# Kernel tuning notes

Hardware: AMD Instinct MI355X
Metric: run time of the kernel (lower is better)

## Reference

```python
import jax, jax.numpy as jnp
import numpy as np

BOX = 8.0  # side length of the box points are sampled in
N_POINTS = 12288
N_BINS_TARGET = 10


def setup_inputs() -> dict:
    key = jax.random.key(0)
    k1, k2 = jax.random.split(key)
    pc = jax.random.uniform(k1, (N_POINTS, 3), dtype=jnp.float32) * BOX
    target_rdf = jax.random.uniform(k2, (N_BINS_TARGET,), dtype=jnp.float32) * 2.0
    return {"reconstructed_pc": pc, "target_rdf": target_rdf, "r_max": 10, "dr": 1.0}


def _calculate_rdf(pc, r_max, dr):
    # pc: [N, 3]. r_max, dr are static Python scalars.
    n = pc.shape[0]
    nbins = int(round(float(r_max) / float(dr)))  # len(arange(0, r_max+dr, dr)) - 1
    # Pairwise Euclidean distances via the Gram-matrix trick (same math as torch.cdist p=2).
    sq = jnp.sum(pc * pc, axis=1)                               # [N]
    d2 = sq[:, None] + sq[None, :] - 2.0 * (pc @ pc.T)          # [N, N]
    d = jnp.sqrt(jnp.maximum(d2, 0.0)).ravel()                  # [N*N]
    # torch.histc(bins=nbins, min=0, max=r_max): uniform bins, max value inclusive in last bin.
    idx = jnp.clip(jnp.floor(d / dr).astype(jnp.int32), 0, nbins - 1)
    w = (d <= r_max).astype(jnp.float32)                        # d >= 0 always holds
    hist = jax.ops.segment_sum(w, idx, num_segments=nbins)      # [nbins]
    r_mid = (jnp.arange(nbins, dtype=jnp.float32) + 0.5) * dr
    density = n / (4.0 / 3.0 * jnp.pi * float(r_max) ** 3)
    ideal_counts = 4.0 * jnp.pi * r_mid ** 2 * dr * density * n
    rdf = hist / ideal_counts
    rdf = jnp.where(jnp.isnan(rdf), 0.0, rdf)
    return rdf, r_mid


def reference(reconstructed_pc, target_rdf, r_max, dr):
    rdf, _ = _calculate_rdf(reconstructed_pc, r_max, dr)
    m = min(int(target_rdf.shape[0]), int(rdf.shape[0]))
    diff = rdf[:m] - target_rdf[:m]
    return jnp.mean(diff * diff)
```

## Files before the change

### kernel.cpp

```cpp
#include <hip/hip_runtime.h>


#define BLOCK    256
#define NB       10
#define SLOT     16
#define FP32_SAT 16777216u

__device__ __forceinline__ int row_start(int r, int T) {
    return r * T - ((r * (r - 1)) >> 1);
}

template <bool DIAG>
__device__ __forceinline__ void tile_loop(const float4* __restrict__ sj,
                                          float sqi, float m2x, float m2y, float m2z,
                                          int tid, unsigned int* c)
{
    for (int jc = 0; jc < BLOCK; jc += 32) {
        unsigned long long cnt = 0ull;
        #pragma unroll
        for (int jj = 0; jj < 32; ++jj) {
            const int j = jc + jj;
            float4 p = sj[j];
            float d2 = sqi + p.w;
            d2 = fmaf(m2x, p.x, d2);
            d2 = fmaf(m2y, p.y, d2);
            d2 = fmaf(m2z, p.z, d2);
            if (DIAG) d2 = (j > tid) ? d2 : 3.0e30f;
            float d = __builtin_amdgcn_sqrtf(d2);
            unsigned int b = (unsigned int)d;
            b = min(b, 10u);
            cnt += 1ull << (b * 6u);
        }
        #pragma unroll
        for (int k = 0; k < NB; ++k)
            c[k] += (unsigned int)(cnt >> (6 * k)) & 63u;
    }
}

__global__ __launch_bounds__(BLOCK) void rdf_hist_kernel(
    const float* __restrict__ pc, const int* __restrict__ rmaxp,
    const float* __restrict__ drp, unsigned int* __restrict__ part,
    int n, int T)
{
    __shared__ float4 sj[BLOCK];
    __shared__ unsigned int sacc[NB];

    const int tid = threadIdx.x;
    const int bid = (int)blockIdx.x;

    const float tf = (float)T;
    float disc = (2.f*tf + 1.f)*(2.f*tf + 1.f) - 8.f*(float)bid;
    int ti = (int)((2.f*tf + 1.f - sqrtf(disc)) * 0.5f);
    ti = max(0, min(ti, T - 1));
    while (ti > 0 && row_start(ti, T) > bid) --ti;
    while (row_start(ti + 1, T) <= bid) ++ti;
    const int tj = ti + (bid - row_start(ti, T));

    const float inv_dr = 1.0f / (*drp);

    if (tid < NB) sacc[tid] = 0u;

    {
        const int j = tj * BLOCK + tid;
        float x = -3.0e4f, y = -3.0e4f, z = -3.0e4f;
        if (j < n) { x = pc[3*j] * inv_dr; y = pc[3*j+1] * inv_dr; z = pc[3*j+2] * inv_dr; }
        sj[tid] = make_float4(x, y, z, x*x + y*y + z*z);
    }
    const int i = ti * BLOCK + tid;
    float xi = 3.0e4f, yi = 3.0e4f, zi = 3.0e4f;
    if (i < n) { xi = pc[3*i] * inv_dr; yi = pc[3*i+1] * inv_dr; zi = pc[3*i+2] * inv_dr; }
    const float sqi = xi*xi + yi*yi + zi*zi;
    const float m2x = -2.f*xi, m2y = -2.f*yi, m2z = -2.f*zi;

    __syncthreads();

    unsigned int c[NB];
    #pragma unroll
    for (int k = 0; k < NB; ++k) c[k] = 0u;

    if (ti == tj) tile_loop<true >(sj, sqi, m2x, m2y, m2z, tid, c);
    else          tile_loop<false>(sj, sqi, m2x, m2y, m2z, tid, c);

    #pragma unroll
    for (int k = 0; k < NB; ++k) {
        unsigned int s = c[k];
        #pragma unroll
        for (int m = 32; m >= 1; m >>= 1) s += (unsigned int)__shfl_xor((int)s, m, 64);
        c[k] = s;
    }
    if ((tid & 63) == 0) {
        #pragma unroll
        for (int k = 0; k < NB; ++k) atomicAdd(&sacc[k], c[k]);
    }
    __syncthreads();
    if (tid < NB) part[bid * SLOT + tid] = sacc[tid];
}

__global__ __launch_bounds__(BLOCK) void rdf_reduce_loss_kernel(
    const unsigned int* __restrict__ part, const float* __restrict__ target,
    const int* __restrict__ rmaxp, const float* __restrict__ drp,
    float* __restrict__ out, int n, int mt, int nblocks)
{
    __shared__ unsigned int sacc[NB];
    const int tid = threadIdx.x;
    if (tid < NB) sacc[tid] = 0u;
    __syncthreads();

    unsigned int a[NB];
    #pragma unroll
    for (int k = 0; k < NB; ++k) a[k] = 0u;
    for (int i = tid; i < nblocks; i += BLOCK) {
        #pragma unroll
        for (int k = 0; k < NB; ++k) a[k] += part[i * SLOT + k];
    }
    #pragma unroll
    for (int k = 0; k < NB; ++k) {
        unsigned int s = a[k];
        #pragma unroll
        for (int m = 32; m >= 1; m >>= 1) s += (unsigned int)__shfl_xor((int)s, m, 64);
        if ((tid & 63) == 0) atomicAdd(&sacc[k], s);
    }
    __syncthreads();

    if (tid == 0) {
        const float PI = 3.14159265358979323846f;
        const float rmax = (float)(*rmaxp);
        const float dr   = *drp;
        int nbins = (int)roundf(rmax / dr);
        if (nbins > NB) nbins = NB;
        const float density = (float)n / (4.0f / 3.0f * PI * rmax * rmax * rmax);
        const int m = (mt < nbins) ? mt : nbins;
        float acc = 0.0f;
        for (int b = 0; b < m; ++b) {
            unsigned int hb = 2u * sacc[b] + ((b == 0) ? (unsigned int)n : 0u);
            if (hb > FP32_SAT) hb = FP32_SAT;
            float r_mid = ((float)b + 0.5f) * dr;
            float ideal = 4.0f * PI * r_mid * r_mid * dr * density * (float)n;
            float rdf  = (ideal != 0.0f) ? ((float)hb / ideal) : 0.0f;
            float diff = rdf - target[b];
            acc = fmaf(diff, diff, acc);
        }
        out[0] = acc / (float)m;
    }
}

extern "C" void kernel_launch(void* const* d_in, const int* in_sizes, int n_in,
                              void* d_out, int out_size, void* d_ws, size_t ws_size,
                              hipStream_t stream)
{
    const float* pc     = (const float*)d_in[0];
    const float* target = (const float*)d_in[1];
    const int*   rmaxp  = (const int*)d_in[2];
    const float* drp    = (const float*)d_in[3];
    const int n  = in_sizes[0] / 3;
    const int mt = in_sizes[1];

    unsigned int* part = (unsigned int*)d_ws;
    const int T = (n + BLOCK - 1) / BLOCK;
    const int nblocks = T * (T + 1) / 2;

    rdf_hist_kernel<<<nblocks, BLOCK, 0, stream>>>(pc, rmaxp, drp, part, n, T);
    rdf_reduce_loss_kernel<<<1, BLOCK, 0, stream>>>(part, target, rmaxp, drp,
                                                    (float*)d_out, n, mt, nblocks);
}
```

Baseline: 40.50 us.

## Register-block four i-points per thread over 2D grid of j-chunks

Each thread now holds four i-points in registers and reuses every shared-memory j-point across them. This cuts LDS reads per pair and amortises the bin-unpack work. The triangular block-index decoding is replaced by a 2D grid of i-tiles (1024 points) by j-chunks (64 points), where blocks below the diagonal exit early. The reduce kernel skips those slots. The trade-off is many tiny blocks (about 2300 launched, roughly half of them empty) and smaller per-block work, which adds launch and reduction overhead and more partial slots.

```diff
diff --git a/kernel.cpp b/kernel.cpp
--- a/kernel.cpp
+++ b/kernel.cpp
@@ -2,34 +2,38 @@
 
 
 #define BLOCK    256
+#define IBLK     4
+#define ITILE    (BLOCK * IBLK)
+#define JCH      64
 #define NB       10
 #define SLOT     16
 #define FP32_SAT 16777216u
 
-__device__ __forceinline__ int row_start(int r, int T) {
-    return r * T - ((r * (r - 1)) >> 1);
-}
-
-template <bool DIAG>
-__device__ __forceinline__ void tile_loop(const float4* __restrict__ sj,
-                                          float sqi, float m2x, float m2y, float m2z,
-                                          int tid, unsigned int* c)
+template <bool STRADDLE>
+__device__ __forceinline__ void jloop(const float4* __restrict__ sj,
+                                      const float* sqi, const float* m2x,
+                                      const float* m2y, const float* m2z,
+                                      const int* iidx, int jbase,
+                                      unsigned int* c)
 {
-    for (int jc = 0; jc < BLOCK; jc += 32) {
+    for (int jc = 0; jc < JCH; jc += 8) {
         unsigned long long cnt = 0ull;
         #pragma unroll
-        for (int jj = 0; jj < 32; ++jj) {
+        for (int jj = 0; jj < 8; ++jj) {
             const int j = jc + jj;
             float4 p = sj[j];
-            float d2 = sqi + p.w;
-            d2 = fmaf(m2x, p.x, d2);
-            d2 = fmaf(m2y, p.y, d2);
-            d2 = fmaf(m2z, p.z, d2);
-            if (DIAG) d2 = (j > tid) ? d2 : 3.0e30f;
-            float d = __builtin_amdgcn_sqrtf(d2);
-            unsigned int b = (unsigned int)d;
-            b = min(b, 10u);
-            cnt += 1ull << (b * 6u);
+            #pragma unroll
+            for (int r = 0; r < IBLK; ++r) {
+                float d2 = sqi[r] + p.w;
+                d2 = fmaf(m2x[r], p.x, d2);
+                d2 = fmaf(m2y[r], p.y, d2);
+                d2 = fmaf(m2z[r], p.z, d2);
+                if (STRADDLE) d2 = (jbase + j > iidx[r]) ? d2 : 3.0e30f;
+                float d = __builtin_amdgcn_sqrtf(d2);
+                unsigned int b = (unsigned int)d;
+                b = min(b, 10u);
+                cnt += 1ull << (b * 6u);
+            }
         }
         #pragma unroll
         for (int k = 0; k < NB; ++k)
@@ -39,38 +43,39 @@
 
 __global__ __launch_bounds__(BLOCK) void rdf_hist_kernel(
     const float* __restrict__ pc, const int* __restrict__ rmaxp,
-    const float* __restrict__ drp, unsigned int* __restrict__ part,
-    int n, int T)
+    const float* __restrict__ drp, unsigned int* __restrict__ part, int n)
 {
-    __shared__ float4 sj[BLOCK];
+    const int I  = (int)blockIdx.x;
+    const int Jc = (int)blockIdx.y;
+    const int jbase = Jc * JCH;
+    const int ibase = I * ITILE;
+    if (jbase + JCH - 1 <= ibase) return;
+
+    __shared__ float4 sj[JCH];
     __shared__ unsigned int sacc[NB];
 
     const int tid = threadIdx.x;
-    const int bid = (int)blockIdx.x;
-
-    const float tf = (float)T;
-    float disc = (2.f*tf + 1.f)*(2.f*tf + 1.f) - 8.f*(float)bid;
-    int ti = (int)((2.f*tf + 1.f - sqrtf(disc)) * 0.5f);
-    ti = max(0, min(ti, T - 1));
-    while (ti > 0 && row_start(ti, T) > bid) --ti;
-    while (row_start(ti + 1, T) <= bid) ++ti;
-    const int tj = ti + (bid - row_start(ti, T));
-
     const float inv_dr = 1.0f / (*drp);
 
     if (tid < NB) sacc[tid] = 0u;
-
-    {
-        const int j = tj * BLOCK + tid;
+    if (tid < JCH) {
+        const int j = jbase + tid;
         float x = -3.0e4f, y = -3.0e4f, z = -3.0e4f;
         if (j < n) { x = pc[3*j] * inv_dr; y = pc[3*j+1] * inv_dr; z = pc[3*j+2] * inv_dr; }
         sj[tid] = make_float4(x, y, z, x*x + y*y + z*z);
     }
-    const int i = ti * BLOCK + tid;
-    float xi = 3.0e4f, yi = 3.0e4f, zi = 3.0e4f;
-    if (i < n) { xi = pc[3*i] * inv_dr; yi = pc[3*i+1] * inv_dr; zi = pc[3*i+2] * inv_dr; }
-    const float sqi = xi*xi + yi*yi + zi*zi;
-    const float m2x = -2.f*xi, m2y = -2.f*yi, m2z = -2.f*zi;
+
+    float sqi[IBLK], m2x[IBLK], m2y[IBLK], m2z[IBLK];
+    int iidx[IBLK];
+    #pragma unroll
+    for (int r = 0; r < IBLK; ++r) {
+        const int i = ibase + tid + BLOCK * r;
+        iidx[r] = i;
+        float x = 3.0e4f, y = 3.0e4f, z = 3.0e4f;
+        if (i < n) { x = pc[3*i] * inv_dr; y = pc[3*i+1] * inv_dr; z = pc[3*i+2] * inv_dr; }
+        sqi[r] = x*x + y*y + z*z;
+        m2x[r] = -2.f * x; m2y[r] = -2.f * y; m2z[r] = -2.f * z;
+    }
 
     __syncthreads();
 
@@ -78,8 +83,10 @@
     #pragma unroll
     for (int k = 0; k < NB; ++k) c[k] = 0u;
 
-    if (ti == tj) tile_loop<true >(sj, sqi, m2x, m2y, m2z, tid, c);
-    else          tile_loop<false>(sj, sqi, m2x, m2y, m2z, tid, c);
+    if (jbase <= ibase + ITILE - 1)
+        jloop<true >(sj, sqi, m2x, m2y, m2z, iidx, jbase, c);
+    else
+        jloop<false>(sj, sqi, m2x, m2y, m2z, iidx, jbase, c);
 
     #pragma unroll
     for (int k = 0; k < NB; ++k) {
@@ -93,13 +100,14 @@
         for (int k = 0; k < NB; ++k) atomicAdd(&sacc[k], c[k]);
     }
     __syncthreads();
+    const int bid = (int)blockIdx.x + (int)gridDim.x * (int)blockIdx.y;
     if (tid < NB) part[bid * SLOT + tid] = sacc[tid];
 }
 
 __global__ __launch_bounds__(BLOCK) void rdf_reduce_loss_kernel(
     const unsigned int* __restrict__ part, const float* __restrict__ target,
     const int* __restrict__ rmaxp, const float* __restrict__ drp,
-    float* __restrict__ out, int n, int mt, int nblocks)
+    float* __restrict__ out, int n, int mt, int nI, int nJ)
 {
     __shared__ unsigned int sacc[NB];
     const int tid = threadIdx.x;
@@ -109,9 +117,14 @@
     unsigned int a[NB];
     #pragma unroll
     for (int k = 0; k < NB; ++k) a[k] = 0u;
-    for (int i = tid; i < nblocks; i += BLOCK) {
-        #pragma unroll
-        for (int k = 0; k < NB; ++k) a[k] += part[i * SLOT + k];
+    const int nslots = nI * nJ;
+    for (int s = tid; s < nslots; s += BLOCK) {
+        const int I  = s % nI;
+        const int Jc = s / nI;
+        if (Jc * JCH + JCH - 1 > I * ITILE) {
+            #pragma unroll
+            for (int k = 0; k < NB; ++k) a[k] += part[s * SLOT + k];
+        }
     }
     #pragma unroll
     for (int k = 0; k < NB; ++k) {
@@ -156,10 +169,11 @@
     const int mt = in_sizes[1];
 
     unsigned int* part = (unsigned int*)d_ws;
-    const int T = (n + BLOCK - 1) / BLOCK;
-    const int nblocks = T * (T + 1) / 2;
+    const int nI = (n + ITILE - 1) / ITILE;
+    const int nJ = (n + JCH - 1) / JCH;
 
-    rdf_hist_kernel<<<nblocks, BLOCK, 0, stream>>>(pc, rmaxp, drp, part, n, T);
+    dim3 grid(nI, nJ);
+    rdf_hist_kernel<<<grid, BLOCK, 0, stream>>>(pc, rmaxp, drp, part, n);
     rdf_reduce_loss_kernel<<<1, BLOCK, 0, stream>>>(part, target, rmaxp, drp,
-                                                    (float*)d_out, n, mt, nblocks);
+                                                    (float*)d_out, n, mt, nI, nJ);
 }
```

Measured after the change: 47.50 us. 17.3% more time.
